# Performance work log

Hardware: AMD Instinct MI355X
Metric: run time of the kernel (lower is better)

Reference implementation:

```python
import jax, jax.numpy as jnp
import numpy as np

N = 100000
E = 1600000
NEG_SLOPE = 0.2
EPS = 1e-16


def gat_layer(x, src, dst, w, W, a_src, a_dst, b):
    # x: [N, Cin] -> h: [N, Cout]
    h = x @ W
    alpha_src = h @ a_src  # [N]
    alpha_dst = h @ a_dst  # [N]
    # per-edge score: alpha_j + alpha_i, leaky relu, edge-weight adjustment
    alpha = alpha_src[src] + alpha_dst[dst]
    alpha = jax.nn.leaky_relu(alpha, NEG_SLOPE)
    alpha = alpha + (1.0 - 1.0 / w)
    # segment softmax over destination nodes
    m = jax.ops.segment_max(alpha, dst, num_segments=N)
    ea = jnp.exp(alpha - m[dst])
    denom = jax.ops.segment_sum(ea, dst, num_segments=N)
    alpha = ea / (denom[dst] + EPS)
    # scatter-add aggregation of weighted source features
    out = jax.ops.segment_sum(h[src] * alpha[:, None], dst, num_segments=N)
    return out + b


def setup_inputs() -> dict:
    key = jax.random.key(0)
    ks = jax.random.split(key, 12)
    return {
        "x": jax.random.normal(ks[0], (N, 128), dtype=jnp.float32),
        "edge_index": jax.random.randint(ks[1], (2, E), 0, N, dtype=jnp.int64)
        if jax.config.jax_enable_x64 else jax.random.randint(ks[1], (2, E), 0, N, dtype=jnp.int32),
        "edge_weight": jax.random.uniform(ks[2], (E,), dtype=jnp.float32, minval=0.5, maxval=1.5),
        "W1": jax.random.normal(ks[3], (128, 64), dtype=jnp.float32) * 0.08,
        "a_src1": jax.random.normal(ks[4], (64,), dtype=jnp.float32) * 0.1,
        "a_dst1": jax.random.normal(ks[5], (64,), dtype=jnp.float32) * 0.1,
        "b1": jax.random.normal(ks[6], (64,), dtype=jnp.float32) * 0.01,
        "W2": jax.random.normal(ks[7], (64, 7), dtype=jnp.float32) * 0.12,
        "a_src2": jax.random.normal(ks[8], (7,), dtype=jnp.float32) * 0.1,
        "a_dst2": jax.random.normal(ks[9], (7,), dtype=jnp.float32) * 0.1,
        "b2": jax.random.normal(ks[10], (7,), dtype=jnp.float32) * 0.01,
    }


def reference(x, edge_index, edge_weight, W1, a_src1, a_dst1, b1, W2, a_src2, a_dst2, b2):
    # add self loops with edge weight fill_value=1.0 (GATConv default behavior)
    loop = jnp.arange(N, dtype=edge_index.dtype)
    src = jnp.concatenate([edge_index[0], loop])
    dst = jnp.concatenate([edge_index[1], loop])
    w = jnp.concatenate([edge_weight, jnp.ones((N,), dtype=edge_weight.dtype)])
    h = gat_layer(x, src, dst, w, W1, a_src1, a_dst1, b1)
    h = jax.nn.relu(h)  # dropout is identity in eval mode
    out = gat_layer(h, src, dst, w, W2, a_src2, a_dst2, b2)
    return out
```

## Files before the change

### kernel.cpp

```cpp
#include <hip/hip_runtime.h>
#include <hip/hip_bf16.h>

typedef __hip_bfloat16 bf16;

#define DEPS 1e-16f
#define CAP 32
#define OVF_MAX 131072

__device__ __forceinline__ float bfu_lo(unsigned u) { return __uint_as_float(u << 16); }
__device__ __forceinline__ float bfu_hi(unsigned u) { return __uint_as_float(u & 0xffff0000u); }

__device__ __forceinline__ float dec_wt(unsigned u) {
    return (float)(u & 32767u) * (1.f / 8192.f) - 1.1f;
}

__global__ __launch_bounds__(256) void f_gemm_hist(
    const float* __restrict__ x, const float* __restrict__ W1,
    const float* __restrict__ a_src, const float* __restrict__ a_dst,
    bf16* __restrict__ h1, float* __restrict__ asrc, float* __restrict__ adst,
    const int* __restrict__ dstv, int* __restrict__ cnt,
    unsigned char* __restrict__ rank8, unsigned* __restrict__ bkt,
    int N, int E, int T, int gG, int gH)
{
    __shared__ __align__(16) float xl[32 * 128];
    int bid = blockIdx.x;
    int r = bid % 13, chunk = bid / 13;
    int tid = threadIdx.x;

    if (r >= 4) {
        int hb = chunk * 9 + (r - 4);
        if (hb >= gH) return;
        int e = hb * 256 + tid;
        if (e >= T) return;
        if (e < E) {
            int d = dstv[e];
            int pos = atomicAdd(&cnt[d], 1);
            rank8[e] = (unsigned char)min(pos, 255);
        } else {
            int d = e - E;
            unsigned q = (unsigned)(1.1f * 8192.f + 0.5f);
            bkt[(size_t)d * CAP] = ((unsigned)d << 15) | q;
        }
        return;
    }
    int gb = chunk * 4 + r;
    if (gb >= gG) return;
    int n0 = gb * 32;
    for (int i = tid; i < 1024; i += 256) {
        int n = n0 + (i >> 5);
        float4 v = {0.f, 0.f, 0.f, 0.f};
        if (n < N) v = ((const float4*)x)[(size_t)n * 32 + (i & 31)];
        ((float4*)xl)[i] = v;
    }
    __syncthreads();
    int w = tid >> 6, c = tid & 63;
    float sa = a_src[c], da = a_dst[c];
    float acc[8] = {0.f, 0.f, 0.f, 0.f, 0.f, 0.f, 0.f, 0.f};
    const float* Wc = W1 + c;
    for (int k4 = 0; k4 < 32; ++k4) {
        float w0 = Wc[(4 * k4 + 0) * 64];
        float w1 = Wc[(4 * k4 + 1) * 64];
        float w2 = Wc[(4 * k4 + 2) * 64];
        float w3 = Wc[(4 * k4 + 3) * 64];
        #pragma unroll
        for (int i = 0; i < 8; ++i) {
            float4 xv = ((const float4*)(xl + (w * 8 + i) * 128))[k4];
            acc[i] = fmaf(xv.x, w0, fmaf(xv.y, w1,
                     fmaf(xv.z, w2, fmaf(xv.w, w3, acc[i]))));
        }
    }
    #pragma unroll
    for (int i = 0; i < 8; ++i) {
        int n = n0 + w * 8 + i;
        float a = acc[i];
        float ps = a * sa, pd = a * da;
        #pragma unroll
        for (int o = 32; o; o >>= 1) {
            ps += __shfl_xor(ps, o);
            pd += __shfl_xor(pd, o);
        }
        if (n < N) {
            h1[(size_t)n * 64 + c] = __float2bfloat16(a);
            if (c == 0) { asrc[n] = ps; adst[n] = pd; }
        }
    }
}

__global__ __launch_bounds__(256) void f_scatB(
    const int* __restrict__ srcv, const int* __restrict__ dstv,
    const float* __restrict__ ew, const unsigned char* __restrict__ rank8,
    unsigned* __restrict__ bkt, uint2* __restrict__ ovf,
    int* __restrict__ ovfn, int E)
{
    int e = blockIdx.x * 256 + threadIdx.x;
    if (e >= E) return;
    int s = srcv[e], d = dstv[e];
    float wt = 1.f - 1.f / ew[e];
    unsigned q = (unsigned)((wt + 1.1f) * 8192.f + 0.5f);
    unsigned entry = ((unsigned)s << 15) | q;
    int pos = 1 + (int)rank8[e];
    if (pos < CAP) {
        bkt[(size_t)d * CAP + pos] = entry;
    } else {
        int o = atomicAdd(ovfn, 1);
        if (o < OVF_MAX) { uint2 v; v.x = (unsigned)d; v.y = entry; ovf[o] = v; }
    }
}

__global__ __launch_bounds__(256) void f_agg1(
    const int* __restrict__ cnt, const unsigned* __restrict__ bkt,
    const uint2* __restrict__ ovf, const int* __restrict__ ovfn,
    const float* __restrict__ asrc, const float* __restrict__ adst,
    const bf16* __restrict__ h1,
    const float* __restrict__ b1, const float* __restrict__ W2,
    const float* __restrict__ a2s, const float* __restrict__ a2d,
    float* __restrict__ h2p, float* __restrict__ ad2, int N)
{
    __shared__ __align__(16) float WxT[16][68];
    __shared__ __align__(16) float b1l[64];
    __shared__ float2 eb[4][64];
    int tid = threadIdx.x;
    if (tid < 64) {
        float us = 0.f, ud = 0.f;
        #pragma unroll
        for (int c = 0; c < 7; ++c) {
            float wv = W2[tid * 7 + c];
            WxT[c][tid] = wv;
            us = fmaf(wv, a2s[c], us);
            ud = fmaf(wv, a2d[c], ud);
        }
        WxT[7][tid] = us;
        WxT[8][tid] = ud;
        #pragma unroll
        for (int r = 9; r < 16; ++r) WxT[r][tid] = 0.f;
        b1l[tid] = b1[tid];
    }
    __syncthreads();
    int d = blockIdx.x * 4 + (tid >> 6);
    int lane = tid & 63;
    if (d >= N) return;
    int lenf = cnt[d] + 1;
    int nc = min(lenf, CAP);
    size_t r0 = (size_t)d * CAP;
    float adv = adst[d];
    int g8 = lane >> 3, l8 = lane & 7;
    float2* ebw = eb[tid >> 6];
    float acc[8] = {0.f, 0.f, 0.f, 0.f, 0.f, 0.f, 0.f, 0.f};
    float sm = 0.f;
    {
        float ea = 0.f; unsigned s = 0;
        if (lane < nc) {
            unsigned u = bkt[r0 + lane];
            s = u >> 15;
            float a = asrc[s] + adv;
            a = (a > 0.f) ? a : 0.2f * a;
            ea = __expf(a + dec_wt(u));
            sm += ea;
        }
        ebw[lane] = make_float2(ea, __uint_as_float(s));
        for (int j = 0; j < nc; j += 8) {
            float2 eq = ebw[j + g8];
            float e = eq.x;
            unsigned sj = __float_as_uint(eq.y);
            uint4 hv = *(const uint4*)&h1[(size_t)sj * 64 + (l8 << 3)];
            acc[0] = fmaf(e, bfu_lo(hv.x), acc[0]);
            acc[1] = fmaf(e, bfu_hi(hv.x), acc[1]);
            acc[2] = fmaf(e, bfu_lo(hv.y), acc[2]);
            acc[3] = fmaf(e, bfu_hi(hv.y), acc[3]);
            acc[4] = fmaf(e, bfu_lo(hv.z), acc[4]);
            acc[5] = fmaf(e, bfu_hi(hv.z), acc[5]);
            acc[6] = fmaf(e, bfu_lo(hv.w), acc[6]);
            acc[7] = fmaf(e, bfu_hi(hv.w), acc[7]);
        }
    }
    if (lenf > CAP) {
        int no = min(*ovfn, OVF_MAX);
        for (int i = g8; i < no; i += 8) {
            uint2 ov = ovf[i];
            if ((int)ov.x == d) {
                unsigned u = ov.y;
                unsigned s = u >> 15;
                float a = asrc[s] + adv;
                a = (a > 0.f) ? a : 0.2f * a;
                float ea = __expf(a + dec_wt(u));
                if (l8 == 0) sm += ea;
                uint4 hv = *(const uint4*)&h1[(size_t)s * 64 + (l8 << 3)];
                acc[0] = fmaf(ea, bfu_lo(hv.x), acc[0]);
                acc[1] = fmaf(ea, bfu_hi(hv.x), acc[1]);
                acc[2] = fmaf(ea, bfu_lo(hv.y), acc[2]);
                acc[3] = fmaf(ea, bfu_hi(hv.y), acc[3]);
                acc[4] = fmaf(ea, bfu_lo(hv.z), acc[4]);
                acc[5] = fmaf(ea, bfu_hi(hv.z), acc[5]);
                acc[6] = fmaf(ea, bfu_lo(hv.w), acc[6]);
                acc[7] = fmaf(ea, bfu_hi(hv.w), acc[7]);
            }
        }
    }
    #pragma unroll
    for (int o = 32; o; o >>= 1) sm += __shfl_xor(sm, o);
    #pragma unroll
    for (int k = 0; k < 8; ++k) {
        acc[k] += __shfl_xor(acc[k], 8);
        acc[k] += __shfl_xor(acc[k], 16);
        acc[k] += __shfl_xor(acc[k], 32);
    }
    float inv = 1.f / (sm + DEPS);
    int c0 = l8 << 3;
    float4 bA = *(const float4*)&b1l[c0];
    float4 bB = *(const float4*)&b1l[c0 + 4];
    float v0 = fmaxf(fmaf(acc[0], inv, bA.x), 0.f);
    float v1 = fmaxf(fmaf(acc[1], inv, bA.y), 0.f);
    float v2 = fmaxf(fmaf(acc[2], inv, bA.z), 0.f);
    float v3 = fmaxf(fmaf(acc[3], inv, bA.w), 0.f);
    float v4 = fmaxf(fmaf(acc[4], inv, bB.x), 0.f);
    float v5 = fmaxf(fmaf(acc[5], inv, bB.y), 0.f);
    float v6 = fmaxf(fmaf(acc[6], inv, bB.z), 0.f);
    float v7 = fmaxf(fmaf(acc[7], inv, bB.w), 0.f);
    float4 wA0 = *(const float4*)&WxT[g8][c0];
    float4 wA1 = *(const float4*)&WxT[g8][c0 + 4];
    float4 wB0 = *(const float4*)&WxT[g8 + 8][c0];
    float4 wB1 = *(const float4*)&WxT[g8 + 8][c0 + 4];
    float rA = fmaf(v0, wA0.x, fmaf(v1, wA0.y, fmaf(v2, wA0.z, fmaf(v3, wA0.w,
               fmaf(v4, wA1.x, fmaf(v5, wA1.y, fmaf(v6, wA1.z, v7 * wA1.w)))))));
    float rB = fmaf(v0, wB0.x, fmaf(v1, wB0.y, fmaf(v2, wB0.z, fmaf(v3, wB0.w,
               fmaf(v4, wB1.x, fmaf(v5, wB1.y, fmaf(v6, wB1.z, v7 * wB1.w)))))));
    rA += __shfl_xor(rA, 1); rA += __shfl_xor(rA, 2); rA += __shfl_xor(rA, 4);
    rB += __shfl_xor(rB, 1); rB += __shfl_xor(rB, 2); rB += __shfl_xor(rB, 4);
    if (l8 == 0) {
        h2p[(size_t)d * 8 + g8] = rA;
        if (g8 == 0) ad2[d] = rB;
    }
}

__global__ __launch_bounds__(256) void f_agg2(
    const int* __restrict__ cnt, const unsigned* __restrict__ bkt,
    const uint2* __restrict__ ovf, const int* __restrict__ ovfn,
    const float* __restrict__ h2p, const float* __restrict__ ad2,
    const float* __restrict__ b2, float* __restrict__ out, int N)
{
    __shared__ float b2l[7];
    if (threadIdx.x < 7) b2l[threadIdx.x] = b2[threadIdx.x];
    __syncthreads();
    int lane = threadIdx.x & 63;
    int wv = threadIdx.x >> 6;
    int grp = lane >> 3, l8 = lane & 7;
    int d = blockIdx.x * 32 + wv * 8 + grp;
    bool valid = d < N;
    int lenf = 0; float adv = 0.f;
    if (valid) { lenf = cnt[d] + 1; adv = ad2[d]; }
    int nc = min(lenf, CAP);
    size_t r0 = (size_t)d * CAP;
    float sm = 0.f;
    float a0 = 0.f, a1 = 0.f, a2 = 0.f, a3 = 0.f, a4 = 0.f, a5 = 0.f, a6 = 0.f;
    for (int p = l8; p < nc; p += 8) {
        unsigned u = bkt[r0 + p];
        int s = (int)(u >> 15);
        const float* hr = &h2p[(size_t)s * 8];
        float4 A = *(const float4*)hr;
        float4 B = *(const float4*)(hr + 4);
        float a = B.w + adv;
        a = (a > 0.f) ? a : 0.2f * a;
        float ea = __expf(a + dec_wt(u));
        sm += ea;
        a0 = fmaf(ea, A.x, a0); a1 = fmaf(ea, A.y, a1);
        a2 = fmaf(ea, A.z, a2); a3 = fmaf(ea, A.w, a3);
        a4 = fmaf(ea, B.x, a4); a5 = fmaf(ea, B.y, a5);
        a6 = fmaf(ea, B.z, a6);
    }
    if (lenf > CAP) {
        int no = min(*ovfn, OVF_MAX);
        for (int i = l8; i < no; i += 8) {
            uint2 ov = ovf[i];
            if ((int)ov.x == d) {
                unsigned u = ov.y;
                int s = (int)(u >> 15);
                const float* hr = &h2p[(size_t)s * 8];
                float4 A = *(const float4*)hr;
                float4 B = *(const float4*)(hr + 4);
                float a = B.w + adv;
                a = (a > 0.f) ? a : 0.2f * a;
                float ea = __expf(a + dec_wt(u));
                sm += ea;
                a0 = fmaf(ea, A.x, a0); a1 = fmaf(ea, A.y, a1);
                a2 = fmaf(ea, A.z, a2); a3 = fmaf(ea, A.w, a3);
                a4 = fmaf(ea, B.x, a4); a5 = fmaf(ea, B.y, a5);
                a6 = fmaf(ea, B.z, a6);
            }
        }
    }
    #pragma unroll
    for (int o = 4; o; o >>= 1) {
        sm += __shfl_xor(sm, o);
        a0 += __shfl_xor(a0, o); a1 += __shfl_xor(a1, o);
        a2 += __shfl_xor(a2, o); a3 += __shfl_xor(a3, o);
        a4 += __shfl_xor(a4, o); a5 += __shfl_xor(a5, o);
        a6 += __shfl_xor(a6, o);
    }
    if (valid && l8 < 7) {
        float inv = 1.f / (sm + DEPS);
        float val = (l8 < 4) ? ((l8 < 2) ? (l8 ? a1 : a0) : ((l8 == 2) ? a2 : a3))
                             : ((l8 < 6) ? ((l8 == 4) ? a4 : a5) : a6);
        out[(size_t)d * 7 + l8] = fmaf(val, inv, b2l[l8]);
    }
}


extern "C" void kernel_launch(void* const* d_in, const int* in_sizes, int n_in,
                              void* d_out, int out_size, void* d_ws, size_t ws_size,
                              hipStream_t stream) {
    const float* x   = (const float*)d_in[0];
    const int*   ei  = (const int*)d_in[1];
    const float* ew  = (const float*)d_in[2];
    const float* W1  = (const float*)d_in[3];
    const float* as1 = (const float*)d_in[4];
    const float* ad1 = (const float*)d_in[5];
    const float* b1  = (const float*)d_in[6];
    const float* W2  = (const float*)d_in[7];
    const float* a2s = (const float*)d_in[8];
    const float* a2d = (const float*)d_in[9];
    const float* b2  = (const float*)d_in[10];

    int N = in_sizes[0] / 128;
    int E = in_sizes[1] / 2;
    int T = E + N;
    const int* srcv = ei;
    const int* dstv = ei + E;
    float* out = (float*)d_out;

    size_t A = 0;
    auto take = [&](size_t b) { size_t o = A; A = (A + b + 255) & ~(size_t)255; return o; };
    size_t o_h1   = take((size_t)N * 64 * 2);
    size_t o_bkt  = take((size_t)N * CAP * 4);
    size_t o_h2p  = take((size_t)N * 8 * 4);
    size_t o_ovf  = take((size_t)OVF_MAX * 8);
    size_t o_cnt  = take((size_t)N * 4);
    size_t o_ovfn = take(256);
    size_t o_asrc = take((size_t)N * 4);
    size_t o_adst = take((size_t)N * 4);
    size_t o_ad2  = take((size_t)N * 4);

    char* base = (char*)d_ws;
    bf16*     h1    = (bf16*)(base + o_h1);
    unsigned* bkt   = (unsigned*)(base + o_bkt);
    float*    h2p   = (float*)(base + o_h2p);
    unsigned char* rank8 = (unsigned char*)(base + o_h2p);
    uint2*    ovf   = (uint2*)(base + o_ovf);
    int*      cnt   = (int*)(base + o_cnt);
    int*      ovfn  = (int*)(base + o_ovfn);
    float*    asrc  = (float*)(base + o_asrc);
    float*    adst  = (float*)(base + o_adst);
    float*    ad2   = (float*)(base + o_ad2);

    int gG = (N + 31) / 32;
    int gH = (T + 255) / 256;
    int chunks = max((gG + 3) / 4, (gH + 8) / 9);
    int gridGH = chunks * 13;
    int gE = (E + 255) / 256;

    hipMemsetAsync(cnt, 0, (size_t)N * 4 + 256, stream);
    f_gemm_hist<<<gridGH, 256, 0, stream>>>(x, W1, as1, ad1, h1, asrc, adst,
                                            dstv, cnt, rank8, bkt, N, E, T, gG, gH);
    f_scatB<<<gE, 256, 0, stream>>>(srcv, dstv, ew, rank8, bkt, ovf, ovfn, E);
    f_agg1 <<<(N + 3) / 4, 256, 0, stream>>>(cnt, bkt, ovf, ovfn, asrc, adst, h1,
                                             b1, W2, a2s, a2d, h2p, ad2, N);
    f_agg2 <<<(N + 31) / 32, 256, 0, stream>>>(cnt, bkt, ovf, ovfn, h2p, ad2, b2, out, N);
}
```

Measured before the change: 287.2 us.

## Fuse edge bucket scatter into histogram pass and batch 8 edges per thread

The separate scatter kernel is merged into the histogram branch of the fused GEMM/histogram kernel. The atomicAdd position is now used directly to write the bucket entry, so the rank8 intermediate array and one kernel launch are gone. Each histogram thread now handles 8 edges with all loads and atomics issued before any stores, which gives more memory-level parallelism. The block interleave ratio between GEMM and histogram blocks changes to 15:4. The cost is more registers and longer-running edge blocks.

```diff
diff --git a/kernel.cpp b/kernel.cpp
--- a/kernel.cpp
+++ b/kernel.cpp
@@ -14,36 +14,62 @@
     return (float)(u & 32767u) * (1.f / 8192.f) - 1.1f;
 }
 
-__global__ __launch_bounds__(256) void f_gemm_hist(
+__global__ __launch_bounds__(256) void f_gemm_hs(
     const float* __restrict__ x, const float* __restrict__ W1,
     const float* __restrict__ a_src, const float* __restrict__ a_dst,
     bf16* __restrict__ h1, float* __restrict__ asrc, float* __restrict__ adst,
-    const int* __restrict__ dstv, int* __restrict__ cnt,
-    unsigned char* __restrict__ rank8, unsigned* __restrict__ bkt,
+    const int* __restrict__ srcv, const int* __restrict__ dstv,
+    const float* __restrict__ ew,
+    int* __restrict__ cnt, unsigned* __restrict__ bkt,
+    uint2* __restrict__ ovf, int* __restrict__ ovfn,
     int N, int E, int T, int gG, int gH)
 {
     __shared__ __align__(16) float xl[32 * 128];
     int bid = blockIdx.x;
-    int r = bid % 13, chunk = bid / 13;
+    int r = bid % 19, chunk = bid / 19;
     int tid = threadIdx.x;
 
-    if (r >= 4) {
-        int hb = chunk * 9 + (r - 4);
+    if (r < 4) {
+        int hb = chunk * 4 + r;
         if (hb >= gH) return;
-        int e = hb * 256 + tid;
-        if (e >= T) return;
-        if (e < E) {
-            int d = dstv[e];
-            int pos = atomicAdd(&cnt[d], 1);
-            rank8[e] = (unsigned char)min(pos, 255);
-        } else {
-            int d = e - E;
-            unsigned q = (unsigned)(1.1f * 8192.f + 0.5f);
-            bkt[(size_t)d * CAP] = ((unsigned)d << 15) | q;
+        int e0 = hb * 2048 + tid;
+        int d_[8], pos_[8], s_[8];
+        float w_[8];
+        #pragma unroll
+        for (int i = 0; i < 8; ++i) {
+            int e = e0 + i * 256;
+            d_[i] = -1; pos_[i] = 0; s_[i] = 0; w_[i] = 1.f;
+            if (e < T) {
+                if (e < E) {
+                    d_[i] = dstv[e];
+                    s_[i] = srcv[e];
+                    w_[i] = ew[e];
+                    pos_[i] = atomicAdd(&cnt[d_[i]], 1);
+                } else {
+                    d_[i] = e - E;
+                    s_[i] = d_[i];
+                    pos_[i] = -1;
+                    w_[i] = -1.f;
+                }
+            }
+        }
+        #pragma unroll
+        for (int i = 0; i < 8; ++i) {
+            if (d_[i] < 0) continue;
+            float wt = (w_[i] < 0.f) ? 0.f : (1.f - 1.f / w_[i]);
+            unsigned q = (unsigned)((wt + 1.1f) * 8192.f + 0.5f);
+            unsigned entry = ((unsigned)s_[i] << 15) | q;
+            int slot = 1 + pos_[i];
+            if (slot < CAP) {
+                bkt[(size_t)d_[i] * CAP + slot] = entry;
+            } else {
+                int o = atomicAdd(ovfn, 1);
+                if (o < OVF_MAX) { uint2 v; v.x = (unsigned)d_[i]; v.y = entry; ovf[o] = v; }
+            }
         }
         return;
     }
-    int gb = chunk * 4 + r;
+    int gb = chunk * 15 + (r - 4);
     if (gb >= gG) return;
     int n0 = gb * 32;
     for (int i = tid; i < 1024; i += 256) {
@@ -83,27 +109,6 @@
             h1[(size_t)n * 64 + c] = __float2bfloat16(a);
             if (c == 0) { asrc[n] = ps; adst[n] = pd; }
         }
-    }
-}
-
-__global__ __launch_bounds__(256) void f_scatB(
-    const int* __restrict__ srcv, const int* __restrict__ dstv,
-    const float* __restrict__ ew, const unsigned char* __restrict__ rank8,
-    unsigned* __restrict__ bkt, uint2* __restrict__ ovf,
-    int* __restrict__ ovfn, int E)
-{
-    int e = blockIdx.x * 256 + threadIdx.x;
-    if (e >= E) return;
-    int s = srcv[e], d = dstv[e];
-    float wt = 1.f - 1.f / ew[e];
-    unsigned q = (unsigned)((wt + 1.1f) * 8192.f + 0.5f);
-    unsigned entry = ((unsigned)s << 15) | q;
-    int pos = 1 + (int)rank8[e];
-    if (pos < CAP) {
-        bkt[(size_t)d * CAP + pos] = entry;
-    } else {
-        int o = atomicAdd(ovfn, 1);
-        if (o < OVF_MAX) { uint2 v; v.x = (unsigned)d; v.y = entry; ovf[o] = v; }
     }
 }
 
@@ -343,7 +348,6 @@
     bf16*     h1    = (bf16*)(base + o_h1);
     unsigned* bkt   = (unsigned*)(base + o_bkt);
     float*    h2p   = (float*)(base + o_h2p);
-    unsigned char* rank8 = (unsigned char*)(base + o_h2p);
     uint2*    ovf   = (uint2*)(base + o_ovf);
     int*      cnt   = (int*)(base + o_cnt);
     int*      ovfn  = (int*)(base + o_ovfn);
@@ -352,15 +356,14 @@
     float*    ad2   = (float*)(base + o_ad2);
 
     int gG = (N + 31) / 32;
-    int gH = (T + 255) / 256;
-    int chunks = max((gG + 3) / 4, (gH + 8) / 9);
-    int gridGH = chunks * 13;
-    int gE = (E + 255) / 256;
+    int gH = (T + 2047) / 2048;
+    int chunks = max((gG + 14) / 15, (gH + 3) / 4);
+    int gridGH = chunks * 19;
 
     hipMemsetAsync(cnt, 0, (size_t)N * 4 + 256, stream);
-    f_gemm_hist<<<gridGH, 256, 0, stream>>>(x, W1, as1, ad1, h1, asrc, adst,
-                                            dstv, cnt, rank8, bkt, N, E, T, gG, gH);
-    f_scatB<<<gE, 256, 0, stream>>>(srcv, dstv, ew, rank8, bkt, ovf, ovfn, E);
+    f_gemm_hs<<<gridGH, 256, 0, stream>>>(x, W1, as1, ad1, h1, asrc, adst,
+                                          srcv, dstv, ew, cnt, bkt, ovf, ovfn,
+                                          N, E, T, gG, gH);
     f_agg1 <<<(N + 3) / 4, 256, 0, stream>>>(cnt, bkt, ovf, ovfn, asrc, adst, h1,
                                              b1, W2, a2s, a2d, h2p, ad2, N);
     f_agg2 <<<(N + 31) / 32, 256, 0, stream>>>(cnt, bkt, ovf, ovfn, h2p, ad2, b2, out, N);
```

After: 271.9 us. -5.3%, faster.
